# Kernel tuning notes

Hardware: AMD Instinct MI355X
Metric: run time of the kernel (lower is better)

Reference implementation:

```python
import jax, jax.numpy as jnp
import numpy as np
import math

B, N, M = 4, 512, 64
F, Q, H, R = 256, 16, 8, 32
D = F // H
ETA = 4.0
EPS = 1e-5
FFN_H = 512

def layer_norm(x, g, b):
    mu = jnp.mean(x, axis=-1, keepdims=True)
    var = jnp.mean((x - mu) ** 2, axis=-1, keepdims=True)
    return (x - mu) * jax.lax.rsqrt(var + EPS) * g + b

def setup_inputs() -> dict:
    key = jax.random.key(0)
    ks = jax.random.split(key, 24)
    def xav(k, shape):
        fan_in, fan_out = shape[1], shape[0]
        std = math.sqrt(2.0 / (fan_in + fan_out))
        return jax.random.normal(k, shape, dtype=jnp.float32) * std
    inp = {
        'a': jax.random.normal(ks[0], (B, N, F), dtype=jnp.float32),
        'charges': jax.random.normal(ks[1], (B, N, Q), dtype=jnp.float32),
        'idx_j': jax.random.randint(ks[2], (B, N, M), 0, N),
        'd_ij': jax.random.uniform(ks[3], (B, N, M), dtype=jnp.float32) * 5.0,
        'mask_ij': jax.random.bernoulli(ks[4], 0.3, (B, N, M)),
        'radial_shifts': jnp.linspace(0.5, 5.0, R, dtype=jnp.float32),
        'Wq': xav(ks[5], (F, F + Q)), 'bq': jnp.zeros((F,), jnp.float32),
        'Wk': xav(ks[6], (F, F + Q)), 'bk': jnp.zeros((F,), jnp.float32),
        'Wv': xav(ks[7], (F, F + Q)), 'bv': jnp.zeros((F,), jnp.float32),
        'Wrb': xav(ks[8], (H, R)), 'brb': jnp.zeros((H,), jnp.float32),
        'Wout': xav(ks[9], (F, 2 * F + R)), 'bout': jnp.zeros((F,), jnp.float32),
        'g1': jnp.ones((F,), jnp.float32), 'b1': jnp.zeros((F,), jnp.float32),
        'g2': jnp.ones((F,), jnp.float32), 'b2': jnp.zeros((F,), jnp.float32),
        'Wf1': xav(ks[10], (FFN_H, F)), 'bf1': jnp.zeros((FFN_H,), jnp.float32),
        'Wf2': xav(ks[11], (F, FFN_H)), 'bf2': jnp.zeros((F,), jnp.float32),
    }
    return inp

def reference(a, charges, idx_j, d_ij, mask_ij, radial_shifts,
              Wq, bq, Wk, bk, Wv, bv, Wrb, brb, Wout, bout,
              g1, b1, g2, b2, Wf1, bf1, Wf2, bf2):
    bidx = jnp.arange(B)[:, None, None]
    a_j = a[bidx, idx_j]          # [B,N,M,F]
    q_j = charges[bidx, idx_j]    # [B,N,M,Q]
    center = jnp.concatenate([a, charges], axis=-1)       # [B,N,F+Q]
    neigh = jnp.concatenate([a_j, q_j], axis=-1)          # [B,N,M,F+Q]
    q = (center @ Wq.T + bq).reshape(B, N, H, D)
    k = (neigh @ Wk.T + bk).reshape(B, N, M, H, D)
    v = (neigh @ Wv.T + bv).reshape(B, N, M, H, D)
    # radial basis: exp(-eta*(d - shift)^2)  -> [B,N,M,R]
    radial = jnp.exp(-ETA * (d_ij[..., None] - radial_shifts) ** 2)
    scores = jnp.einsum('bnhd,bnmhd->bnmh', q, k) / math.sqrt(D)
    scores = scores + radial @ Wrb.T + brb                # [B,N,M,H]
    scores = jnp.swapaxes(scores, -1, -2)                 # [B,N,H,M]
    scores = jnp.where(mask_ij[:, :, None, :], -jnp.inf, scores)
    attn = jax.nn.softmax(scores, axis=-1)
    attn = jnp.nan_to_num(attn, nan=0.0, posinf=0.0, neginf=0.0)
    context = jnp.einsum('bnhm,bnmhd->bnhd', attn, v).reshape(B, N, F)
    radial_context = jnp.einsum('bnhm,bnmg->bnhg', attn, radial).mean(axis=-2)  # [B,N,R]
    update = jnp.concatenate([a, context, radial_context], axis=-1) @ Wout.T + bout
    x = layer_norm(a + update, g1, b1)
    ff = jax.nn.gelu(x @ Wf1.T + bf1, approximate=False) @ Wf2.T + bf2
    return layer_norm(x + ff, g2, b2)
```

## Files before the change

### kernel.cpp

```cpp
#include <hip/hip_runtime.h>
#include <hip/hip_bf16.h>
#include <math.h>

#define Bb 4
#define Nn 512
#define Mm 64
#define Ff 256
#define Qq 16
#define Hh 8
#define Rr 32
#define FFNH 512
#define ROWS (Bb*Nn)
#define KIN (Ff+Qq)
#define KINP 288
#define KOUT (2*Ff+Rr)

typedef short short8 __attribute__((ext_vector_type(8)));
typedef float f32x4 __attribute__((ext_vector_type(4)));

__device__ inline unsigned short f2b(float f) {
    union { float f; unsigned u; } c; c.f = f;
    unsigned r = c.u + 0x7fffu + ((c.u >> 16) & 1u);
    return (unsigned short)(r >> 16);
}

#define OFF_CENTER 0
#define OFF_WQKV   (OFF_CENTER + ROWS*KINP)
#define OFF_WOUT   (OFF_WQKV + 768*KINP)
#define OFF_WF1    (OFF_WOUT + Ff*KOUT)
#define OFF_WF2    (OFF_WF1 + FFNH*Ff)
#define OFF_U      (OFF_WF2 + Ff*FFNH)
#define OFF_XB     (OFF_U + ROWS*KOUT)
#define OFF_FFH    (OFF_XB + ROWS*Ff)
#define CONV_TOTAL OFF_U
#define CONV_BLK   (CONV_TOTAL/256)
#define A2U_BLK    (ROWS*Ff/256)
#define MSK_BLK    (Bb*Nn*Mm/256)

__global__ __launch_bounds__(256) void prep(const float* __restrict__ a,
                                            const float* __restrict__ ch,
                                            const float* __restrict__ Wq,
                                            const float* __restrict__ Wk,
                                            const float* __restrict__ Wv,
                                            const float* __restrict__ Wout,
                                            const float* __restrict__ Wf1,
                                            const float* __restrict__ Wf2,
                                            const unsigned char* __restrict__ mask,
                                            int* __restrict__ flag,
                                            unsigned short* __restrict__ arena) {
    int bid = blockIdx.x, tid = threadIdx.x;
    if (bid < CONV_BLK) {
        int i = bid * 256 + tid;
        float v;
        if (i < OFF_WQKV) {
            int row = i / KINP, c = i - row * KINP;
            v = (c < Ff) ? a[(size_t)row * Ff + c] : (c < KIN ? ch[(size_t)row * Qq + (c - Ff)] : 0.f);
        } else if (i < OFF_WOUT) {
            int j = i - OFF_WQKV;
            int n = j / KINP, c = j - n * KINP;
            const float* W = n < 256 ? Wq : (n < 512 ? Wk : Wv);
            int nr = n & 255;
            v = (c < KIN) ? W[(size_t)nr * KIN + c] : 0.f;
        } else if (i < OFF_WF1) {
            v = Wout[i - OFF_WOUT];
        } else if (i < OFF_WF2) {
            v = Wf1[i - OFF_WF1];
        } else {
            v = Wf2[i - OFF_WF2];
        }
        arena[i] = f2b(v);
    } else if (bid < CONV_BLK + A2U_BLK) {
        int j = (bid - CONV_BLK) * 256 + tid;
        int row = j >> 8, col = j & 255;
        arena[OFF_U + (size_t)row * KOUT + col] = f2b(a[j]);
    } else {
        int i = (bid - CONV_BLK - A2U_BLK) * 256 + tid;
        if ((i & 3) && mask[i]) *flag = 1;
    }
}

template<int KT, int SPLIT, int MODE>
__global__ __launch_bounds__(256) void gemm_mfma(const unsigned short* __restrict__ Ab, int lda,
                                                 const unsigned short* __restrict__ Wb, int ldw,
                                                 const float* __restrict__ b0,
                                                 const float* __restrict__ b1,
                                                 const float* __restrict__ b2,
                                                 float* __restrict__ C,
                                                 unsigned short* __restrict__ Cb,
                                                 int ldc, size_t pstride) {
    __shared__ unsigned short As[2][64][32];
    __shared__ unsigned short Bs[2][64][32];
    int tid = threadIdx.x;
    int colbase = blockIdx.x * 64;
    int rowbase = blockIdx.y * 64;
    constexpr int TPER = (KT + SPLIT - 1) / SPLIT;
    int t0 = blockIdx.z * TPER;
    int NL = KT - t0; if (NL > TPER) NL = TPER;

    int sr = tid >> 2, sl = tid & 3;
    const unsigned short* Ap = Ab + (size_t)(rowbase + sr) * lda + sl * 8;
    const unsigned short* Wp = Wb + (size_t)(colbase + sr) * ldw + sl * 8;
    int ssw = (sl ^ (sr & 3)) * 8;

    int wave = tid >> 6, lane = tid & 63;
    int wr = (wave >> 1) * 32, wc = (wave & 1) * 32;
    int lrow = lane & 15;
    int kslot = lane >> 4;
    int sp = (kslot ^ (lane & 3)) * 8;

    uint4 av, wv;
    auto prefetch = [&](int t) {
        av = *reinterpret_cast<const uint4*>(Ap + (size_t)t * 32);
        wv = *reinterpret_cast<const uint4*>(Wp + (size_t)t * 32);
    };
    auto writeLDS = [&](int buf) {
        *reinterpret_cast<uint4*>(&As[buf][sr][ssw]) = av;
        *reinterpret_cast<uint4*>(&Bs[buf][sr][ssw]) = wv;
    };

    f32x4 acc[2][2] = {};
    prefetch(t0);
    writeLDS(0);
    __syncthreads();
    for (int tt = 0; tt < NL; ++tt) {
        if (tt + 1 < NL) prefetch(t0 + tt + 1);
        int buf = tt & 1;
        short8 a0 = *reinterpret_cast<const short8*>(&As[buf][wr + lrow][sp]);
        short8 a1 = *reinterpret_cast<const short8*>(&As[buf][wr + 16 + lrow][sp]);
        short8 bv0 = *reinterpret_cast<const short8*>(&Bs[buf][wc + lrow][sp]);
        short8 bv1 = *reinterpret_cast<const short8*>(&Bs[buf][wc + 16 + lrow][sp]);
        acc[0][0] = __builtin_amdgcn_mfma_f32_16x16x32_bf16(a0, bv0, acc[0][0], 0, 0, 0);
        acc[0][1] = __builtin_amdgcn_mfma_f32_16x16x32_bf16(a0, bv1, acc[0][1], 0, 0, 0);
        acc[1][0] = __builtin_amdgcn_mfma_f32_16x16x32_bf16(a1, bv0, acc[1][0], 0, 0, 0);
        acc[1][1] = __builtin_amdgcn_mfma_f32_16x16x32_bf16(a1, bv1, acc[1][1], 0, 0, 0);
        if (tt + 1 < NL) {
            writeLDS((tt + 1) & 1);
            __syncthreads();
        }
    }

    const float* bias = b0;
    if (MODE == 1) {
        int sel = colbase >> 8;
        bias = sel == 0 ? b0 : (sel == 1 ? b1 : b2);
    }
    int colq = (colbase & 255);
    float* Cp = (MODE == 0) ? C + (size_t)blockIdx.z * pstride : C;
    #pragma unroll
    for (int fr = 0; fr < 2; ++fr) {
        #pragma unroll
        for (int fc = 0; fc < 2; ++fc) {
            int coll = wc + fc * 16 + (lane & 15);
            int col = colbase + coll;
            #pragma unroll
            for (int i = 0; i < 4; ++i) {
                int row = rowbase + wr + fr * 16 + (lane >> 4) * 4 + i;
                float v = acc[fr][fc][i];
                if (MODE == 0) {
                    Cp[(size_t)row * ldc + col] = v;
                } else if (MODE == 1) {
                    Cp[(size_t)row * ldc + col] = v + bias[colq + coll];
                } else {
                    v += bias[col];
                    v = 0.5f * v * (1.0f + erff(v * 0.70710678118654752f));
                    Cb[(size_t)row * ldc + col] = f2b(v);
                }
            }
        }
    }
}

__global__ __launch_bounds__(256) void attn_kernel(const float* __restrict__ QKV,
                                                   const int* __restrict__ idx_j,
                                                   const float* __restrict__ d_ij,
                                                   const void* __restrict__ mask,
                                                   const float* __restrict__ shifts,
                                                   const float* __restrict__ Wrb,
                                                   const float* __restrict__ brb,
                                                   const int* __restrict__ flag,
                                                   unsigned short* __restrict__ Ub) {
    __shared__ float Ktile[16][260];
    __shared__ float rad[Mm][36];
    __shared__ float att[Hh][Mm];
    __shared__ float attbar[Mm];
    __shared__ int   jl[Mm];
    __shared__ float dv[Mm];
    __shared__ int   maskf[Mm];
    __shared__ float shs[Rr];

    int row = blockIdx.x;
    int b = row >> 9;
    int tid = threadIdx.x;
    bool boolmask = (*flag != 0);

    if (tid < Mm) jl[tid] = idx_j[row * Mm + tid];
    else if (tid < 128) { int m = tid - 64; dv[m] = d_ij[row * Mm + m]; }
    else if (tid < 160) shs[tid - 128] = shifts[tid - 128];
    else if (tid >= 192) {
        int m = tid - 192;
        maskf[m] = boolmask ? (int)((const unsigned char*)mask)[row * Mm + m]
                            : ((const int*)mask)[row * Mm + m];
    }

    int half = tid & 1;
    int p = tid >> 1;
    int hh = p >> 4;
    int ml = p & 15;
    float4 qreg[4], wreg[4];
    #pragma unroll
    for (int c = 0; c < 4; ++c) {
        qreg[c] = *reinterpret_cast<const float4*>(QKV + (size_t)row * 768 + hh * 32 + half * 16 + c * 4);
        wreg[c] = *reinterpret_cast<const float4*>(Wrb + hh * Rr + half * 16 + c * 4);
    }
    float brbh = brb[hh];
    __syncthreads();

    int sw = tid >> 6, sl = tid & 63;
    int rloc = sw * 4 + (sl >> 4);
    int scol = sl & 15;
    auto stage = [&](int t, int seg) {
        int j = jl[t * 16 + rloc];
        const float4* src = reinterpret_cast<const float4*>(QKV + (size_t)(b * Nn + j) * 768 + seg);
        #pragma unroll
        for (int c = 0; c < 4; ++c) {
            float4 v = src[c * 16 + scol];
            *reinterpret_cast<float4*>(&Ktile[rloc][c * 64 + scol * 4]) = v;
        }
    };

    #pragma unroll
    for (int it = 0; it < 8; ++it) {
        int i = tid + it * 256;
        int m = i >> 5, r = i & 31;
        float t = dv[m] - shs[r];
        rad[m][r] = expf(-4.0f * t * t);
    }
    stage(0, 256);
    __syncthreads();

    for (int t = 0; t < 4; ++t) {
        float accK = 0.f, accR = 0.f;
        #pragma unroll
        for (int c = 0; c < 4; ++c) {
            float4 kv = *reinterpret_cast<const float4*>(&Ktile[ml][hh * 32 + half * 16 + c * 4]);
            accK += qreg[c].x * kv.x + qreg[c].y * kv.y + qreg[c].z * kv.z + qreg[c].w * kv.w;
            float4 rv = *reinterpret_cast<const float4*>(&rad[t * 16 + ml][half * 16 + c * 4]);
            accR += wreg[c].x * rv.x + wreg[c].y * rv.y + wreg[c].z * rv.z + wreg[c].w * rv.w;
        }
        float tv = accK * 0.17677669529663687f + accR;
        tv += __shfl_xor(tv, 1);
        if (!half) {
            int m = t * 16 + ml;
            att[hh][m] = maskf[m] ? -INFINITY : (tv + brbh);
        }
        __syncthreads();
        if (t < 3) { stage(t + 1, 256); __syncthreads(); }
    }

    {
        int h = tid >> 5, l = tid & 31;
        float s0 = att[h][l], s1 = att[h][l + 32];
        float mx = fmaxf(s0, s1);
        #pragma unroll
        for (int off = 16; off; off >>= 1) mx = fmaxf(mx, __shfl_xor(mx, off, 32));
        float e0 = 0.f, e1 = 0.f;
        if (mx != -INFINITY) {
            e0 = expf(s0 - mx);
            e1 = expf(s1 - mx);
        }
        float sm = e0 + e1;
        #pragma unroll
        for (int off = 16; off; off >>= 1) sm += __shfl_xor(sm, off, 32);
        float inv = sm > 0.f ? 1.f / sm : 0.f;
        att[h][l] = e0 * inv;
        att[h][l + 32] = e1 * inv;
    }
    __syncthreads();

    if (tid < Mm) {
        float sv = 0.f;
        #pragma unroll
        for (int h = 0; h < Hh; ++h) sv += att[h][tid];
        attbar[tid] = sv * 0.125f;
    }
    stage(0, 512);
    __syncthreads();

    float ctx = 0.f;
    int h2 = tid >> 5, d0 = tid & 31;
    for (int t = 0; t < 4; ++t) {
        #pragma unroll
        for (int m = 0; m < 16; ++m)
            ctx = fmaf(att[h2][t * 16 + m], Ktile[m][h2 * 32 + d0], ctx);
        __syncthreads();
        if (t < 3) { stage(t + 1, 512); __syncthreads(); }
    }

    Ub[(size_t)row * KOUT + Ff + tid] = f2b(ctx);

    if (tid < 64) {
        int g = tid >> 1;
        float acc = 0.f;
        #pragma unroll
        for (int i = 0; i < 32; ++i) {
            int m = half * 32 + i;
            acc = fmaf(attbar[m], rad[m][g], acc);
        }
        acc += __shfl_xor(acc, 1);
        if (!half) Ub[(size_t)row * KOUT + 2 * Ff + g] = f2b(acc);
    }
}

template<int S, int WB>
__global__ __launch_bounds__(256) void add_ln_c(const float* __restrict__ x0,
                                                const float* __restrict__ part, size_t pstride,
                                                const float* __restrict__ bias,
                                                const float* __restrict__ g,
                                                const float* __restrict__ be,
                                                float* __restrict__ outp,
                                                unsigned short* __restrict__ xb) {
    int tid = threadIdx.x;
    int wave = tid >> 6, lane = tid & 63;
    int row = blockIdx.x * 4 + wave;
    size_t off = (size_t)row * Ff + lane * 4;
    float4 v = *reinterpret_cast<const float4*>(x0 + off);
    float4 bb = *reinterpret_cast<const float4*>(bias + lane * 4);
    v.x += bb.x; v.y += bb.y; v.z += bb.z; v.w += bb.w;
    #pragma unroll
    for (int s = 0; s < S; ++s) {
        float4 p = *reinterpret_cast<const float4*>(part + (size_t)s * pstride + off);
        v.x += p.x; v.y += p.y; v.z += p.z; v.w += p.w;
    }
    float sm = v.x + v.y + v.z + v.w;
    #pragma unroll
    for (int o = 32; o; o >>= 1) sm += __shfl_xor(sm, o, 64);
    float mu = sm * (1.f / Ff);
    float4 c = {v.x - mu, v.y - mu, v.z - mu, v.w - mu};
    float s2 = c.x * c.x + c.y * c.y + c.z * c.z + c.w * c.w;
    #pragma unroll
    for (int o = 32; o; o >>= 1) s2 += __shfl_xor(s2, o, 64);
    float inv = rsqrtf(s2 * (1.f / Ff) + 1e-5f);
    float4 gg = *reinterpret_cast<const float4*>(g + lane * 4);
    float4 ee = *reinterpret_cast<const float4*>(be + lane * 4);
    float4 r;
    r.x = c.x * inv * gg.x + ee.x;
    r.y = c.y * inv * gg.y + ee.y;
    r.z = c.z * inv * gg.z + ee.z;
    r.w = c.w * inv * gg.w + ee.w;
    *reinterpret_cast<float4*>(outp + off) = r;
    if (WB) {
        ushort4 u;
        u.x = f2b(r.x); u.y = f2b(r.y); u.z = f2b(r.z); u.w = f2b(r.w);
        *reinterpret_cast<ushort4*>(&xb[off]) = u;
    }
}

extern "C" void kernel_launch(void* const* d_in, const int* in_sizes, int n_in,
                              void* d_out, int out_size, void* d_ws, size_t ws_size,
                              hipStream_t stream) {
    const float* a       = (const float*)d_in[0];
    const float* charges = (const float*)d_in[1];
    const int*   idx_j   = (const int*)  d_in[2];
    const float* d_ij    = (const float*)d_in[3];
    const void*  mask    =               d_in[4];
    const float* shifts  = (const float*)d_in[5];
    const float* Wq   = (const float*)d_in[6];  const float* bq   = (const float*)d_in[7];
    const float* Wk   = (const float*)d_in[8];  const float* bk   = (const float*)d_in[9];
    const float* Wv   = (const float*)d_in[10]; const float* bv   = (const float*)d_in[11];
    const float* Wrb  = (const float*)d_in[12]; const float* brb  = (const float*)d_in[13];
    const float* Wout = (const float*)d_in[14]; const float* bout = (const float*)d_in[15];
    const float* g1   = (const float*)d_in[16]; const float* b1   = (const float*)d_in[17];
    const float* g2   = (const float*)d_in[18]; const float* b2   = (const float*)d_in[19];
    const float* Wf1  = (const float*)d_in[20]; const float* bf1  = (const float*)d_in[21];
    const float* Wf2  = (const float*)d_in[22]; const float* bf2  = (const float*)d_in[23];
    float* outp = (float*)d_out;

    float* ws   = (float*)d_ws;
    int*   flag = (int*)d_ws;
    float* QKVb = ws + 1024;
    float* part = QKVb;
    float* xbuf = QKVb + 2097152;
    unsigned short* arena = (unsigned short*)(xbuf + (size_t)ROWS * Ff);
    unsigned short* centerb = arena + OFF_CENTER;
    unsigned short* Wqkvb   = arena + OFF_WQKV;
    unsigned short* Woutb   = arena + OFF_WOUT;
    unsigned short* Wf1b    = arena + OFF_WF1;
    unsigned short* Wf2b    = arena + OFF_WF2;
    unsigned short* Ub      = arena + OFF_U;
    unsigned short* xb      = arena + OFF_XB;
    unsigned short* ffhb    = arena + OFF_FFH;

    hipMemsetAsync(flag, 0, sizeof(int), stream);
    prep<<<CONV_BLK + A2U_BLK + MSK_BLK, 256, 0, stream>>>(
        a, charges, Wq, Wk, Wv, Wout, Wf1, Wf2, (const unsigned char*)mask, flag, arena);

    gemm_mfma<9, 1, 1><<<dim3(12, 32, 1), 256, 0, stream>>>(
        centerb, KINP, Wqkvb, KINP, bq, bk, bv, QKVb, nullptr, 768, 0);

    attn_kernel<<<ROWS, 256, 0, stream>>>(QKVb, idx_j, d_ij, mask, shifts, Wrb, brb, flag, Ub);

    gemm_mfma<17, 2, 0><<<dim3(4, 32, 2), 256, 0, stream>>>(
        Ub, KOUT, Woutb, KOUT, nullptr, nullptr, nullptr, part, nullptr, Ff, (size_t)ROWS * Ff);
    add_ln_c<2, 1><<<ROWS / 4, 256, 0, stream>>>(a, part, (size_t)ROWS * Ff, bout, g1, b1, xbuf, xb);

    gemm_mfma<8, 1, 2><<<dim3(8, 32, 1), 256, 0, stream>>>(
        xb, Ff, Wf1b, Ff, bf1, nullptr, nullptr, nullptr, ffhb, FFNH, 0);

    gemm_mfma<16, 2, 0><<<dim3(4, 32, 2), 256, 0, stream>>>(
        ffhb, FFNH, Wf2b, FFNH, nullptr, nullptr, nullptr, part, nullptr, Ff, (size_t)ROWS * Ff);
    add_ln_c<2, 0><<<ROWS / 4, 256, 0, stream>>>(xbuf, part, (size_t)ROWS * Ff, bf2, g2, b2, outp, nullptr);
}
```

Measured before the change: 73.93 us.

## Store QKV in bf16 and double-buffer neighbor K/V tiles in attention

The QKV projection now writes bf16 instead of fp32, and the attention kernel gathers neighbor K/V rows as bf16, halving gather traffic and shared-memory footprint. The K/V staging is double-buffered so the next tile's gather overlaps compute on the current one, which removes one barrier per iteration. The attbar reduction is folded into the first context iteration. Rounding K/V/Q to bf16 adds some numerical error to the scores and context.

```diff
diff --git a/kernel.cpp b/kernel.cpp
--- a/kernel.cpp
+++ b/kernel.cpp
@@ -16,12 +16,17 @@
 #define KOUT (2*Ff+Rr)
 
 typedef short short8 __attribute__((ext_vector_type(8)));
+typedef unsigned short ushort8 __attribute__((ext_vector_type(8)));
 typedef float f32x4 __attribute__((ext_vector_type(4)));
 
 __device__ inline unsigned short f2b(float f) {
     union { float f; unsigned u; } c; c.f = f;
     unsigned r = c.u + 0x7fffu + ((c.u >> 16) & 1u);
     return (unsigned short)(r >> 16);
+}
+__device__ inline float b2f(unsigned short u) {
+    union { unsigned u; float f; } c; c.u = ((unsigned)u) << 16;
+    return c.f;
 }
 
 #define OFF_CENTER 0
@@ -32,6 +37,7 @@
 #define OFF_U      (OFF_WF2 + Ff*FFNH)
 #define OFF_XB     (OFF_U + ROWS*KOUT)
 #define OFF_FFH    (OFF_XB + ROWS*Ff)
+#define OFF_QKVB   (OFF_FFH + ROWS*FFNH)
 #define CONV_TOTAL OFF_U
 #define CONV_BLK   (CONV_TOTAL/256)
 #define A2U_BLK    (ROWS*Ff/256)
@@ -159,7 +165,7 @@
                 if (MODE == 0) {
                     Cp[(size_t)row * ldc + col] = v;
                 } else if (MODE == 1) {
-                    Cp[(size_t)row * ldc + col] = v + bias[colq + coll];
+                    Cb[(size_t)row * ldc + col] = f2b(v + bias[colq + coll]);
                 } else {
                     v += bias[col];
                     v = 0.5f * v * (1.0f + erff(v * 0.70710678118654752f));
@@ -170,7 +176,7 @@
     }
 }
 
-__global__ __launch_bounds__(256) void attn_kernel(const float* __restrict__ QKV,
+__global__ __launch_bounds__(256) void attn_kernel(const unsigned short* __restrict__ QKV,
                                                    const int* __restrict__ idx_j,
                                                    const float* __restrict__ d_ij,
                                                    const void* __restrict__ mask,
@@ -179,7 +185,7 @@
                                                    const float* __restrict__ brb,
                                                    const int* __restrict__ flag,
                                                    unsigned short* __restrict__ Ub) {
-    __shared__ float Ktile[16][260];
+    __shared__ unsigned short Kt[2][16][280];
     __shared__ float rad[Mm][36];
     __shared__ float att[Hh][Mm];
     __shared__ float attbar[Mm];
@@ -206,25 +212,30 @@
     int p = tid >> 1;
     int hh = p >> 4;
     int ml = p & 15;
-    float4 qreg[4], wreg[4];
-    #pragma unroll
-    for (int c = 0; c < 4; ++c) {
-        qreg[c] = *reinterpret_cast<const float4*>(QKV + (size_t)row * 768 + hh * 32 + half * 16 + c * 4);
+    float qf[16];
+    {
+        const unsigned short* qrow = QKV + (size_t)row * 768 + hh * 32 + half * 16;
+        ushort8 q0 = *reinterpret_cast<const ushort8*>(qrow);
+        ushort8 q1 = *reinterpret_cast<const ushort8*>(qrow + 8);
+        #pragma unroll
+        for (int i = 0; i < 8; ++i) { qf[i] = b2f(q0[i]); qf[8 + i] = b2f(q1[i]); }
+    }
+    float4 wreg[4];
+    #pragma unroll
+    for (int c = 0; c < 4; ++c)
         wreg[c] = *reinterpret_cast<const float4*>(Wrb + hh * Rr + half * 16 + c * 4);
-    }
     float brbh = brb[hh];
     __syncthreads();
 
-    int sw = tid >> 6, sl = tid & 63;
-    int rloc = sw * 4 + (sl >> 4);
-    int scol = sl & 15;
-    auto stage = [&](int t, int seg) {
-        int j = jl[t * 16 + rloc];
-        const float4* src = reinterpret_cast<const float4*>(QKV + (size_t)(b * Nn + j) * 768 + seg);
-        #pragma unroll
-        for (int c = 0; c < 4; ++c) {
-            float4 v = src[c * 16 + scol];
-            *reinterpret_cast<float4*>(&Ktile[rloc][c * 64 + scol * 4]) = v;
+    auto stage = [&](int t, int seg, int buf) {
+        #pragma unroll
+        for (int q = 0; q < 2; ++q) {
+            int chunk = q * 256 + tid;
+            int r = chunk >> 5, s = chunk & 31;
+            int j = jl[t * 16 + r];
+            const uint4* src = reinterpret_cast<const uint4*>(QKV + (size_t)(b * Nn + j) * 768 + seg);
+            uint4 v = src[s];
+            *reinterpret_cast<uint4*>(&Kt[buf][r][s * 8]) = v;
         }
     };
 
@@ -235,15 +246,23 @@
         float t = dv[m] - shs[r];
         rad[m][r] = expf(-4.0f * t * t);
     }
-    stage(0, 256);
+    stage(0, 256, 0);
     __syncthreads();
 
     for (int t = 0; t < 4; ++t) {
-        float accK = 0.f, accR = 0.f;
+        if (t < 3) stage(t + 1, 256, (t + 1) & 1);
+        int buf = t & 1;
+        const unsigned short* kr = &Kt[buf][ml][hh * 32 + half * 16];
+        ushort8 k0 = *reinterpret_cast<const ushort8*>(kr);
+        ushort8 k1 = *reinterpret_cast<const ushort8*>(kr + 8);
+        float accK = 0.f;
+        #pragma unroll
+        for (int i = 0; i < 8; ++i) accK = fmaf(qf[i], b2f(k0[i]), accK);
+        #pragma unroll
+        for (int i = 0; i < 8; ++i) accK = fmaf(qf[8 + i], b2f(k1[i]), accK);
+        float accR = 0.f;
         #pragma unroll
         for (int c = 0; c < 4; ++c) {
-            float4 kv = *reinterpret_cast<const float4*>(&Ktile[ml][hh * 32 + half * 16 + c * 4]);
-            accK += qreg[c].x * kv.x + qreg[c].y * kv.y + qreg[c].z * kv.z + qreg[c].w * kv.w;
             float4 rv = *reinterpret_cast<const float4*>(&rad[t * 16 + ml][half * 16 + c * 4]);
             accR += wreg[c].x * rv.x + wreg[c].y * rv.y + wreg[c].z * rv.z + wreg[c].w * rv.w;
         }
@@ -254,7 +273,6 @@
             att[hh][m] = maskf[m] ? -INFINITY : (tv + brbh);
         }
         __syncthreads();
-        if (t < 3) { stage(t + 1, 256); __syncthreads(); }
     }
 
     {
@@ -275,25 +293,24 @@
         att[h][l] = e0 * inv;
         att[h][l + 32] = e1 * inv;
     }
-    __syncthreads();
-
-    if (tid < Mm) {
-        float sv = 0.f;
-        #pragma unroll
-        for (int h = 0; h < Hh; ++h) sv += att[h][tid];
-        attbar[tid] = sv * 0.125f;
-    }
-    stage(0, 512);
+    stage(0, 512, 0);
     __syncthreads();
 
     float ctx = 0.f;
     int h2 = tid >> 5, d0 = tid & 31;
     for (int t = 0; t < 4; ++t) {
+        if (t < 3) stage(t + 1, 512, (t + 1) & 1);
+        int buf = t & 1;
         #pragma unroll
         for (int m = 0; m < 16; ++m)
-            ctx = fmaf(att[h2][t * 16 + m], Ktile[m][h2 * 32 + d0], ctx);
+            ctx = fmaf(att[h2][t * 16 + m], b2f(Kt[buf][m][h2 * 32 + d0]), ctx);
+        if (t == 0 && tid < Mm) {
+            float sv = 0.f;
+            #pragma unroll
+            for (int h = 0; h < Hh; ++h) sv += att[h][tid];
+            attbar[tid] = sv * 0.125f;
+        }
         __syncthreads();
-        if (t < 3) { stage(t + 1, 512); __syncthreads(); }
     }
 
     Ub[(size_t)row * KOUT + Ff + tid] = f2b(ctx);
@@ -377,10 +394,9 @@
 
     float* ws   = (float*)d_ws;
     int*   flag = (int*)d_ws;
-    float* QKVb = ws + 1024;
-    float* part = QKVb;
-    float* xbuf = QKVb + 2097152;
-    unsigned short* arena = (unsigned short*)(xbuf + (size_t)ROWS * Ff);
+    float* part = ws + 1024;
+    float* xbuf = part + 1048576;
+    unsigned short* arena = (unsigned short*)(xbuf + 524288);
     unsigned short* centerb = arena + OFF_CENTER;
     unsigned short* Wqkvb   = arena + OFF_WQKV;
     unsigned short* Woutb   = arena + OFF_WOUT;
@@ -389,15 +405,16 @@
     unsigned short* Ub      = arena + OFF_U;
     unsigned short* xb      = arena + OFF_XB;
     unsigned short* ffhb    = arena + OFF_FFH;
+    unsigned short* QKVB16  = arena + OFF_QKVB;
 
     hipMemsetAsync(flag, 0, sizeof(int), stream);
     prep<<<CONV_BLK + A2U_BLK + MSK_BLK, 256, 0, stream>>>(
         a, charges, Wq, Wk, Wv, Wout, Wf1, Wf2, (const unsigned char*)mask, flag, arena);
 
     gemm_mfma<9, 1, 1><<<dim3(12, 32, 1), 256, 0, stream>>>(
-        centerb, KINP, Wqkvb, KINP, bq, bk, bv, QKVb, nullptr, 768, 0);
-
-    attn_kernel<<<ROWS, 256, 0, stream>>>(QKVb, idx_j, d_ij, mask, shifts, Wrb, brb, flag, Ub);
+        centerb, KINP, Wqkvb, KINP, bq, bk, bv, nullptr, QKVB16, 768, 0);
+
+    attn_kernel<<<ROWS, 256, 0, stream>>>(QKVB16, idx_j, d_ij, mask, shifts, Wrb, brb, flag, Ub);
 
     gemm_mfma<17, 2, 0><<<dim3(4, 32, 2), 256, 0, stream>>>(
         Ub, KOUT, Woutb, KOUT, nullptr, nullptr, nullptr, part, nullptr, Ff, (size_t)ROWS * Ff);
```

Measured after the change: 65.64 us. 11.2% less time.
